# Kernel optimization log

Measured on AMD Instinct MI355X. Metric: run time of the kernel, lower is better.

## Reference

```python
import jax, jax.numpy as jnp
import numpy as np

N_HEAD = 16


def setup_inputs() -> dict:
    key = jax.random.key(0)
    k1, k2, k3 = jax.random.split(key, 3)
    B, T, C = 4, 2048, 1024
    x = jax.random.normal(k1, (B, T, C), dtype=jnp.float32)
    Wqkv = jax.random.normal(k2, (C, 3 * C), dtype=jnp.float32) * 0.02
    Wproj = jax.random.normal(k3, (C, C), dtype=jnp.float32) * 0.02
    return {"x": x, "Wqkv": Wqkv, "Wproj": Wproj}


def reference(x, Wqkv, Wproj):
    B, T, C = x.shape
    nh = N_HEAD
    hd = C // nh
    qkv = x @ Wqkv                                  # (B, T, 3C)
    q, k, v = jnp.split(qkv, 3, axis=-1)
    # (B, T, C) -> (B, nh, T, hd)
    q = q.reshape(B, T, nh, hd).transpose(0, 2, 1, 3)
    k = k.reshape(B, T, nh, hd).transpose(0, 2, 1, 3)
    v = v.reshape(B, T, nh, hd).transpose(0, 2, 1, 3)
    # scaled dot-product attention with causal mask (past_kv=None => T_all == T)
    att = jnp.einsum("bhtd,bhsd->bhts", q, k) / jnp.sqrt(jnp.float32(hd))
    causal = jnp.tril(jnp.ones((T, T), dtype=bool))  # (T, T)
    att = jnp.where(causal[None, None, :, :], att, jnp.float32(-jnp.inf))
    att = jax.nn.softmax(att, axis=-1)              # (B, nh, T, T)
    y = jnp.einsum("bhts,bhsd->bhtd", att, v)       # (B, nh, T, hd)
    y = y.transpose(0, 2, 1, 3).reshape(B, T, C)
    y = y @ Wproj                                   # (B, T, C)
    # present_kv (detached in original)
    return y, jax.lax.stop_gradient(k), jax.lax.stop_gradient(v)
```

## Files before the change

### kernel.cpp

```cpp
#include <hip/hip_runtime.h>
#include <hip/hip_bf16.h>


typedef __bf16 bf16;
typedef __attribute__((ext_vector_type(8))) __bf16 bf16x8;
typedef __attribute__((ext_vector_type(4))) __bf16 bf16x4;
typedef __attribute__((ext_vector_type(4))) float f32x4;

#define AS_G __attribute__((address_space(1)))
#define AS_L __attribute__((address_space(3)))

#define QSCALE 0.1803368801111204f

__device__ __forceinline__ void gld_lds16(const bf16* g, bf16* l) {
  __builtin_amdgcn_global_load_lds((const AS_G void*)g, (AS_L void*)l, 16, 0, 0);
}

__global__ __launch_bounds__(256) void k_cast(const float* __restrict__ in,
                                              bf16* __restrict__ out, int n) {
  int i = (blockIdx.x * 256 + threadIdx.x) * 8;
  if (i >= n) return;
  float4 a = *(const float4*)(in + i);
  float4 b = *(const float4*)(in + i + 4);
  bf16x8 o;
  o[0] = (bf16)a.x; o[1] = (bf16)a.y; o[2] = (bf16)a.z; o[3] = (bf16)a.w;
  o[4] = (bf16)b.x; o[5] = (bf16)b.y; o[6] = (bf16)b.z; o[7] = (bf16)b.w;
  *(bf16x8*)(out + i) = o;
}

__global__ __launch_bounds__(256) void k_transpose(const float* __restrict__ in,
                                                   bf16* __restrict__ out,
                                                   int K, int N) {
  __shared__ float tile[32][33];
  int bx = blockIdx.x * 32;
  int by = blockIdx.y * 32;
  int tx = threadIdx.x, ty = threadIdx.y;
#pragma unroll
  for (int i = 0; i < 4; ++i)
    tile[ty + i * 8][tx] = in[(size_t)(by + ty + i * 8) * N + bx + tx];
  __syncthreads();
#pragma unroll
  for (int i = 0; i < 4; ++i)
    out[(size_t)(bx + ty + i * 8) * K + by + tx] = (bf16)tile[tx][ty + i * 8];
}

__device__ __forceinline__ void gemm_tile_128(const bf16* __restrict__ A,
                                              const bf16* __restrict__ Bt,
                                              int m0, int n0,
                                              bf16* As, bf16* Bs,
                                              f32x4 acc[4][4]) {
  const int tid = threadIdx.x;
  const int w = tid >> 6, lane = tid & 63, lo = lane & 15, hi = lane >> 4;
  const int wm = w >> 1, wn = w & 1;
#pragma unroll 1
  for (int k0 = 0; k0 < 1024; k0 += 32) {
#pragma unroll
    for (int p = 0; p < 2; ++p) {
      int u = tid + 256 * p;
      int row = u >> 2, cs = u & 3;
      int g = cs ^ ((row >> 1) & 3);
      gld_lds16(A + (size_t)(m0 + row) * 1024 + k0 + g * 8, As + p * 2048 + w * 512);
      gld_lds16(Bt + (size_t)(n0 + row) * 1024 + k0 + g * 8, Bs + p * 2048 + w * 512);
    }
    __syncthreads();
    bf16x8 af[4], bfr[4];
#pragma unroll
    for (int i = 0; i < 4; ++i) {
      int row = wm * 64 + i * 16 + lo;
      af[i] = *(const bf16x8*)(As + row * 32 + (hi ^ ((row >> 1) & 3)) * 8);
    }
#pragma unroll
    for (int j = 0; j < 4; ++j) {
      int row = wn * 64 + j * 16 + lo;
      bfr[j] = *(const bf16x8*)(Bs + row * 32 + (hi ^ ((row >> 1) & 3)) * 8);
    }
#pragma unroll
    for (int i = 0; i < 4; ++i)
#pragma unroll
      for (int j = 0; j < 4; ++j)
        acc[i][j] = __builtin_amdgcn_mfma_f32_16x16x32_bf16(af[i], bfr[j], acc[i][j], 0, 0, 0);
    __syncthreads();
  }
}

__global__ __launch_bounds__(256) void k_gemm_qkv(const bf16* __restrict__ x,
                                                  const bf16* __restrict__ WqkvT,
                                                  bf16* __restrict__ qb, bf16* __restrict__ kb,
                                                  bf16* __restrict__ vtb,
                                                  float* __restrict__ outk, float* __restrict__ outv) {
  __shared__ bf16 As[128 * 32], Bs[128 * 32];
  f32x4 acc[4][4] = {};
  int m0 = blockIdx.y * 128, n0 = blockIdx.x * 128;
  gemm_tile_128(x, WqkvT, m0, n0, As, Bs, acc);
  const int tid = threadIdx.x;
  const int w = tid >> 6, lane = tid & 63, lo = lane & 15, hi = lane >> 4;
  const int wm = w >> 1, wn = w & 1;
#pragma unroll
  for (int i = 0; i < 4; ++i) {
    int growbase = m0 + wm * 64 + i * 16 + hi * 4;
    int b = growbase >> 11, t0 = growbase & 2047;
#pragma unroll
    for (int j = 0; j < 4; ++j) {
      int gcol = n0 + wn * 64 + j * 16 + lo;
      int part = gcol >> 10;
      int cc = gcol & 1023, h = cc >> 6, d = cc & 63;
      size_t idx0 = ((size_t)(b * 16 + h) * 2048 + t0) * 64 + d;
      if (part == 0) {
#pragma unroll
        for (int r = 0; r < 4; ++r) qb[idx0 + (size_t)r * 64] = (bf16)(acc[i][j][r] * QSCALE);
      } else if (part == 1) {
#pragma unroll
        for (int r = 0; r < 4; ++r) {
          float val = acc[i][j][r];
          kb[idx0 + (size_t)r * 64] = (bf16)val;
          outk[idx0 + (size_t)r * 64] = val;
        }
      } else {
        bf16x4 pk;
#pragma unroll
        for (int r = 0; r < 4; ++r) {
          float val = acc[i][j][r];
          outv[idx0 + (size_t)r * 64] = val;
          pk[r] = (bf16)val;
        }
        *(bf16x4*)(vtb + ((size_t)(b * 16 + h) * 64 + d) * 2048 + t0) = pk;
      }
    }
  }
}

__global__ __launch_bounds__(256) void k_gemm_proj(const bf16* __restrict__ yb,
                                                   const bf16* __restrict__ WprojT,
                                                   float* __restrict__ out) {
  __shared__ bf16 As[128 * 32], Bs[128 * 32];
  f32x4 acc[4][4] = {};
  int m0 = blockIdx.y * 128, n0 = blockIdx.x * 128;
  gemm_tile_128(yb, WprojT, m0, n0, As, Bs, acc);
  const int tid = threadIdx.x;
  const int w = tid >> 6, lane = tid & 63, lo = lane & 15, hi = lane >> 4;
  const int wm = w >> 1, wn = w & 1;
#pragma unroll
  for (int i = 0; i < 4; ++i)
#pragma unroll
    for (int j = 0; j < 4; ++j)
#pragma unroll
      for (int r = 0; r < 4; ++r) {
        int grow = m0 + wm * 64 + i * 16 + hi * 4 + r;
        int gcol = n0 + wn * 64 + j * 16 + lo;
        out[(size_t)grow * 1024 + gcol] = acc[i][j][r];
      }
}

__device__ __forceinline__ void p_store(f32x4 sacc[4], bool mask,
                                        int w, int lo, int hi, bf16* psrow) {
  if (mask) {
#pragma unroll
    for (int nt = 0; nt < 4; ++nt)
#pragma unroll
      for (int r = 0; r < 4; ++r)
        if (nt * 16 + hi * 4 + r > w * 16 + lo) sacc[nt][r] = -1e30f;
  }
#pragma unroll
  for (int nt = 0; nt < 4; ++nt) {
    bf16x4 pk;
#pragma unroll
    for (int r = 0; r < 4; ++r) pk[r] = (bf16)exp2f(sacc[nt][r]);
    *(bf16x4*)(psrow + (w * 16 + lo) * 72 + nt * 16 + hi * 4) = pk;
  }
}

__device__ __forceinline__ void write_y(bf16* __restrict__ y, int b, int h, int qrow,
                                        int hi, const f32x4 o[4], float inv) {
  size_t base = ((size_t)b * 2048 + qrow) * 1024 + h * 64;
#pragma unroll
  for (int mt = 0; mt < 4; ++mt) {
    bf16x4 yk;
#pragma unroll
    for (int r = 0; r < 4; ++r) yk[r] = (bf16)(o[mt][r] * inv);
    *(bf16x4*)(y + base + mt * 16 + hi * 4) = yk;
  }
}

__global__ __launch_bounds__(256, 4) void k_flash(const bf16* __restrict__ q,
                                                  const bf16* __restrict__ k,
                                                  const bf16* __restrict__ vt,
                                                  bf16* __restrict__ y) {
  __shared__ bf16 Ks[64 * 64];
  __shared__ bf16 Vs[80 * 64];
  __shared__ bf16 Ps[128 * 72];
  const int bi = blockIdx.x;
  const int slot = bi >> 3;
  const int bh = (bi & 7) + 8 * (slot >> 4);
  const int j = slot & 15;
  const int jA = j, jB = 31 - j;
  const int tid = threadIdx.x, w = tid >> 6, lane = tid & 63, lo = lane & 15, hi = lane >> 4;
  const bf16* qp = q + (size_t)bh * 2048 * 64;
  const bf16* kp = k + (size_t)bh * 2048 * 64;
  const bf16* vtp = vt + (size_t)bh * 64 * 2048;

  {
    int rr = tid >> 4, c = (tid & 15) * 4;
    bf16x4 z;
    bf16 v1 = (rr == 0) ? (bf16)1.0f : (bf16)0.0f;
    z[0] = v1; z[1] = v1; z[2] = v1; z[3] = v1;
    *(bf16x4*)(Vs + (64 + rr) * 64 + c) = z;
  }

  bf16x8 qfA[2], qfB[2];
  {
    int qA = jA * 64 + w * 16 + lo;
    int qB = jB * 64 + w * 16 + lo;
    qfA[0] = *(const bf16x8*)(qp + (size_t)qA * 64 + hi * 8);
    qfA[1] = *(const bf16x8*)(qp + (size_t)qA * 64 + 32 + hi * 8);
    qfB[0] = *(const bf16x8*)(qp + (size_t)qB * 64 + hi * 8);
    qfB[1] = *(const bf16x8*)(qp + (size_t)qB * 64 + 32 + hi * 8);
  }
  f32x4 oA[4] = {}, oB[4] = {};
  f32x4 oLA = {}, oLB = {};

  for (int st = 0; st <= jB; ++st) {
    const int s0 = st * 64;
#pragma unroll
    for (int p = 0; p < 2; ++p) {
      int u = tid + 256 * p;
      int row = u >> 3, c = u & 7, g = c ^ (row & 7);
      gld_lds16(kp + (size_t)(s0 + row) * 64 + g * 8, Ks + p * 2048 + w * 512);
      gld_lds16(vtp + (size_t)row * 2048 + s0 + g * 8, Vs + p * 2048 + w * 512);
    }
    __syncthreads();

    bf16x8 kf[4][2];
#pragma unroll
    for (int nt = 0; nt < 4; ++nt)
#pragma unroll
      for (int ks = 0; ks < 2; ++ks)
        kf[nt][ks] = *(const bf16x8*)(Ks + (nt * 16 + lo) * 64 + ((ks * 4 + hi) ^ (lo & 7)) * 8);

    const bool actA = (st <= jA);
    if (actA) {
      f32x4 sacc[4] = {};
#pragma unroll
      for (int nt = 0; nt < 4; ++nt)
#pragma unroll
        for (int ks = 0; ks < 2; ++ks)
          sacc[nt] = __builtin_amdgcn_mfma_f32_16x16x32_bf16(kf[nt][ks], qfA[ks], sacc[nt], 0, 0, 0);
      p_store(sacc, st == jA, w, lo, hi, Ps);
    }
    {
      f32x4 sacc[4] = {};
#pragma unroll
      for (int nt = 0; nt < 4; ++nt)
#pragma unroll
        for (int ks = 0; ks < 2; ++ks)
          sacc[nt] = __builtin_amdgcn_mfma_f32_16x16x32_bf16(kf[nt][ks], qfB[ks], sacc[nt], 0, 0, 0);
      p_store(sacc, st == jB, w, lo, hi, Ps + 64 * 72);
    }
    __asm__ volatile("s_waitcnt lgkmcnt(0)" ::: "memory");

    bf16x8 pfA[2], pfB[2];
#pragma unroll
    for (int ks = 0; ks < 2; ++ks) {
      pfB[ks] = *(const bf16x8*)(Ps + (64 + w * 16 + lo) * 72 + ks * 32 + hi * 8);
      if (actA) pfA[ks] = *(const bf16x8*)(Ps + (w * 16 + lo) * 72 + ks * 32 + hi * 8);
    }
#pragma unroll
    for (int mt = 0; mt < 5; ++mt) {
#pragma unroll
      for (int ks = 0; ks < 2; ++ks) {
        int row = mt * 16 + lo;
        bf16x8 vf = *(const bf16x8*)(Vs + row * 64 + ((ks * 4 + hi) ^ (row & 7)) * 8);
        if (mt < 4) {
          oB[mt] = __builtin_amdgcn_mfma_f32_16x16x32_bf16(vf, pfB[ks], oB[mt], 0, 0, 0);
          if (actA) oA[mt] = __builtin_amdgcn_mfma_f32_16x16x32_bf16(vf, pfA[ks], oA[mt], 0, 0, 0);
        } else {
          oLB = __builtin_amdgcn_mfma_f32_16x16x32_bf16(vf, pfB[ks], oLB, 0, 0, 0);
          if (actA) oLA = __builtin_amdgcn_mfma_f32_16x16x32_bf16(vf, pfA[ks], oLA, 0, 0, 0);
        }
      }
    }
    __syncthreads();
  }

  const int b = bh >> 4, h = bh & 15;
  float lA = __shfl(oLA[0], lo, 64);
  float lB = __shfl(oLB[0], lo, 64);
  write_y(y, b, h, jA * 64 + w * 16 + lo, hi, oA, 1.0f / lA);
  write_y(y, b, h, jB * 64 + w * 16 + lo, hi, oB, 1.0f / lB);
}

extern "C" void kernel_launch(void* const* d_in, const int* in_sizes, int n_in,
                              void* d_out, int out_size, void* d_ws, size_t ws_size,
                              hipStream_t stream) {
  const float* x = (const float*)d_in[0];
  const float* Wqkv = (const float*)d_in[1];
  const float* Wproj = (const float*)d_in[2];
  float* out = (float*)d_out;

  const size_t YSZ = (size_t)8192 * 1024;
  char* ws = (char*)d_ws;
  bf16* xb = (bf16*)ws;      ws += (size_t)8192 * 1024 * 2;
  bf16* wqkvT = (bf16*)ws;   ws += (size_t)3072 * 1024 * 2;
  bf16* wprojT = (bf16*)ws;  ws += (size_t)1024 * 1024 * 2;
  bf16* qb = (bf16*)ws;      ws += (size_t)64 * 2048 * 64 * 2;
  bf16* kb = (bf16*)ws;      ws += (size_t)64 * 2048 * 64 * 2;
  bf16* vtb = (bf16*)ws;     ws += (size_t)64 * 2048 * 64 * 2;
  bf16* yb = (bf16*)ws;

  float* outy = out;
  float* outk = out + YSZ;
  float* outv = out + 2 * YSZ;

  k_cast<<<4096, 256, 0, stream>>>(x, xb, 8388608);
  dim3 tb(32, 8);
  k_transpose<<<dim3(96, 32), tb, 0, stream>>>(Wqkv, wqkvT, 1024, 3072);
  k_transpose<<<dim3(32, 32), tb, 0, stream>>>(Wproj, wprojT, 1024, 1024);
  k_gemm_qkv<<<dim3(24, 64), 256, 0, stream>>>(xb, wqkvT, qb, kb, vtb, outk, outv);
  k_flash<<<1024, 256, 0, stream>>>(qb, kb, vtb, yb);
  k_gemm_proj<<<dim3(8, 64), 256, 0, stream>>>(yb, wprojT, outy);
}
```

Before: 324.3 us.

## Use 256x256 triple-buffered GEMM tiles and tweak flash attention P layout

Both projection GEMMs switch to 512-thread blocks computing 256x256 tiles. They use a three-stage LDS pipeline with split A/B prefetch, MFMA priority raising and an XCD-aware block swizzle, which raises data reuse and hides global load latency. The flash kernel pads the P scratch stride to cut LDS bank conflicts, uses the hardware exp2 builtin, and issues both score MFMA batches before the exp/stores. Bigger tiles leave the proj GEMM with only 128 blocks, which risks underfilling the GPU.

```diff
diff --git a/kernel.cpp b/kernel.cpp
--- a/kernel.cpp
+++ b/kernel.cpp
@@ -44,74 +44,112 @@
     out[(size_t)(bx + ty + i * 8) * K + by + tx] = (bf16)tile[tx][ty + i * 8];
 }
 
-__device__ __forceinline__ void gemm_tile_128(const bf16* __restrict__ A,
+__device__ __forceinline__ void gemm_main_256(const bf16* __restrict__ A,
                                               const bf16* __restrict__ Bt,
                                               int m0, int n0,
                                               bf16* As, bf16* Bs,
-                                              f32x4 acc[4][4]) {
+                                              f32x4 acc[8][4]) {
   const int tid = threadIdx.x;
   const int w = tid >> 6, lane = tid & 63, lo = lane & 15, hi = lane >> 4;
-  const int wm = w >> 1, wn = w & 1;
+  const int wm = w >> 2, wn = w & 3;
+  const int r0 = tid >> 2;
+  const int g = (tid & 3) ^ (r0 & 3) ^ ((r0 >> 2) & 3);
+  const bf16* ga = A + (size_t)(m0 + r0) * 1024 + g * 8;
+  const bf16* gb = Bt + (size_t)(n0 + r0) * 1024 + g * 8;
+
+#define STAGE_A(t, i) do { \
+    gld_lds16(ga + (t) * 32, As + (i) * 8192 + w * 512); \
+    gld_lds16(ga + 131072 + (t) * 32, As + (i) * 8192 + 4096 + w * 512); } while (0)
+#define STAGE_B(t, i) do { \
+    gld_lds16(gb + (t) * 32, Bs + (i) * 8192 + w * 512); \
+    gld_lds16(gb + 131072 + (t) * 32, Bs + (i) * 8192 + 4096 + w * 512); } while (0)
+
+  STAGE_A(0, 0); STAGE_B(0, 0);
+  STAGE_A(1, 1); STAGE_B(1, 1);
+
+  bf16x8 a[4], b[4];
 #pragma unroll 1
-  for (int k0 = 0; k0 < 1024; k0 += 32) {
-#pragma unroll
-    for (int p = 0; p < 2; ++p) {
-      int u = tid + 256 * p;
-      int row = u >> 2, cs = u & 3;
-      int g = cs ^ ((row >> 1) & 3);
-      gld_lds16(A + (size_t)(m0 + row) * 1024 + k0 + g * 8, As + p * 2048 + w * 512);
-      gld_lds16(Bt + (size_t)(n0 + row) * 1024 + k0 + g * 8, Bs + p * 2048 + w * 512);
-    }
-    __syncthreads();
-    bf16x8 af[4], bfr[4];
-#pragma unroll
-    for (int i = 0; i < 4; ++i) {
-      int row = wm * 64 + i * 16 + lo;
-      af[i] = *(const bf16x8*)(As + row * 32 + (hi ^ ((row >> 1) & 3)) * 8);
-    }
-#pragma unroll
-    for (int j = 0; j < 4; ++j) {
-      int row = wn * 64 + j * 16 + lo;
-      bfr[j] = *(const bf16x8*)(Bs + row * 32 + (hi ^ ((row >> 1) & 3)) * 8);
-    }
-#pragma unroll
-    for (int i = 0; i < 4; ++i)
-#pragma unroll
-      for (int j = 0; j < 4; ++j)
-        acc[i][j] = __builtin_amdgcn_mfma_f32_16x16x32_bf16(af[i], bfr[j], acc[i][j], 0, 0, 0);
-    __syncthreads();
-  }
-}
-
-__global__ __launch_bounds__(256) void k_gemm_qkv(const bf16* __restrict__ x,
-                                                  const bf16* __restrict__ WqkvT,
-                                                  bf16* __restrict__ qb, bf16* __restrict__ kb,
-                                                  bf16* __restrict__ vtb,
-                                                  float* __restrict__ outk, float* __restrict__ outv) {
-  __shared__ bf16 As[128 * 32], Bs[128 * 32];
-  f32x4 acc[4][4] = {};
-  int m0 = blockIdx.y * 128, n0 = blockIdx.x * 128;
-  gemm_tile_128(x, WqkvT, m0, n0, As, Bs, acc);
+  for (int t = 0; t < 32; ++t) {
+    if (t < 31) asm volatile("s_waitcnt vmcnt(4)" ::: "memory");
+    else        asm volatile("s_waitcnt vmcnt(0)" ::: "memory");
+    __builtin_amdgcn_s_barrier();
+    const int buf = t % 3;
+    const int sbuf = (t + 2) % 3;
+    const bf16* Ab = As + buf * 8192;
+    const bf16* Bb = Bs + buf * 8192;
+
+#pragma unroll
+    for (int mi = 0; mi < 4; ++mi) {
+      int r = wm * 128 + mi * 16 + lo;
+      a[mi] = *(const bf16x8*)(Ab + r * 32 + (hi ^ (r & 3) ^ ((r >> 2) & 3)) * 8);
+    }
+#pragma unroll
+    for (int ni = 0; ni < 4; ++ni) {
+      int r = wn * 64 + ni * 16 + lo;
+      b[ni] = *(const bf16x8*)(Bb + r * 32 + (hi ^ (r & 3) ^ ((r >> 2) & 3)) * 8);
+    }
+    if (t < 30) STAGE_A(t + 2, sbuf);
+    __builtin_amdgcn_s_barrier();
+    __builtin_amdgcn_s_setprio(1);
+#pragma unroll
+    for (int mi = 0; mi < 4; ++mi)
+#pragma unroll
+      for (int ni = 0; ni < 4; ++ni)
+        acc[mi][ni] = __builtin_amdgcn_mfma_f32_16x16x32_bf16(a[mi], b[ni], acc[mi][ni], 0, 0, 0);
+    __builtin_amdgcn_s_setprio(0);
+    __builtin_amdgcn_s_barrier();
+
+#pragma unroll
+    for (int mi = 0; mi < 4; ++mi) {
+      int r = wm * 128 + 64 + mi * 16 + lo;
+      a[mi] = *(const bf16x8*)(Ab + r * 32 + (hi ^ (r & 3) ^ ((r >> 2) & 3)) * 8);
+    }
+    if (t < 30) STAGE_B(t + 2, sbuf);
+    __builtin_amdgcn_s_barrier();
+    __builtin_amdgcn_s_setprio(1);
+#pragma unroll
+    for (int mi = 0; mi < 4; ++mi)
+#pragma unroll
+      for (int ni = 0; ni < 4; ++ni)
+        acc[4 + mi][ni] = __builtin_amdgcn_mfma_f32_16x16x32_bf16(a[mi], b[ni], acc[4 + mi][ni], 0, 0, 0);
+    __builtin_amdgcn_s_setprio(0);
+  }
+#undef STAGE_A
+#undef STAGE_B
+}
+
+__global__ __launch_bounds__(512, 2) void k_gemm_qkv(const bf16* __restrict__ x,
+                                                     const bf16* __restrict__ WqkvT,
+                                                     bf16* __restrict__ qb, bf16* __restrict__ kb,
+                                                     bf16* __restrict__ vtb,
+                                                     float* __restrict__ outk, float* __restrict__ outv) {
+  __shared__ bf16 As[3 * 8192], Bs[3 * 8192];
+  int id = blockIdx.x;
+  int swz = (id & 7) * 48 + (id >> 3);
+  int by = swz / 12, bx = swz - by * 12;
+  int m0 = by * 256, n0 = bx * 256;
+  f32x4 acc[8][4] = {};
+  gemm_main_256(x, WqkvT, m0, n0, As, Bs, acc);
   const int tid = threadIdx.x;
   const int w = tid >> 6, lane = tid & 63, lo = lane & 15, hi = lane >> 4;
-  const int wm = w >> 1, wn = w & 1;
-#pragma unroll
-  for (int i = 0; i < 4; ++i) {
-    int growbase = m0 + wm * 64 + i * 16 + hi * 4;
-    int b = growbase >> 11, t0 = growbase & 2047;
-#pragma unroll
-    for (int j = 0; j < 4; ++j) {
-      int gcol = n0 + wn * 64 + j * 16 + lo;
+  const int wm = w >> 2, wn = w & 3;
+#pragma unroll
+  for (int mi = 0; mi < 8; ++mi) {
+    int growbase = m0 + wm * 128 + mi * 16 + hi * 4;
+    int bb = growbase >> 11, t0 = growbase & 2047;
+#pragma unroll
+    for (int ni = 0; ni < 4; ++ni) {
+      int gcol = n0 + wn * 64 + ni * 16 + lo;
       int part = gcol >> 10;
       int cc = gcol & 1023, h = cc >> 6, d = cc & 63;
-      size_t idx0 = ((size_t)(b * 16 + h) * 2048 + t0) * 64 + d;
+      size_t idx0 = ((size_t)(bb * 16 + h) * 2048 + t0) * 64 + d;
       if (part == 0) {
 #pragma unroll
-        for (int r = 0; r < 4; ++r) qb[idx0 + (size_t)r * 64] = (bf16)(acc[i][j][r] * QSCALE);
+        for (int r = 0; r < 4; ++r) qb[idx0 + (size_t)r * 64] = (bf16)(acc[mi][ni][r] * QSCALE);
       } else if (part == 1) {
 #pragma unroll
         for (int r = 0; r < 4; ++r) {
-          float val = acc[i][j][r];
+          float val = acc[mi][ni][r];
           kb[idx0 + (size_t)r * 64] = (bf16)val;
           outk[idx0 + (size_t)r * 64] = val;
         }
@@ -119,37 +157,42 @@
         bf16x4 pk;
 #pragma unroll
         for (int r = 0; r < 4; ++r) {
-          float val = acc[i][j][r];
+          float val = acc[mi][ni][r];
           outv[idx0 + (size_t)r * 64] = val;
           pk[r] = (bf16)val;
         }
-        *(bf16x4*)(vtb + ((size_t)(b * 16 + h) * 64 + d) * 2048 + t0) = pk;
+        *(bf16x4*)(vtb + ((size_t)(bb * 16 + h) * 64 + d) * 2048 + t0) = pk;
       }
     }
   }
 }
 
-__global__ __launch_bounds__(256) void k_gemm_proj(const bf16* __restrict__ yb,
-                                                   const bf16* __restrict__ WprojT,
-                                                   float* __restrict__ out) {
-  __shared__ bf16 As[128 * 32], Bs[128 * 32];
-  f32x4 acc[4][4] = {};
-  int m0 = blockIdx.y * 128, n0 = blockIdx.x * 128;
-  gemm_tile_128(yb, WprojT, m0, n0, As, Bs, acc);
+__global__ __launch_bounds__(512, 2) void k_gemm_proj(const bf16* __restrict__ yb,
+                                                      const bf16* __restrict__ WprojT,
+                                                      float* __restrict__ out) {
+  __shared__ bf16 As[3 * 8192], Bs[3 * 8192];
+  int id = blockIdx.x;
+  int swz = (id & 7) * 16 + (id >> 3);
+  int by = swz >> 2, bx = swz & 3;
+  int m0 = by * 256, n0 = bx * 256;
+  f32x4 acc[8][4] = {};
+  gemm_main_256(yb, WprojT, m0, n0, As, Bs, acc);
   const int tid = threadIdx.x;
   const int w = tid >> 6, lane = tid & 63, lo = lane & 15, hi = lane >> 4;
-  const int wm = w >> 1, wn = w & 1;
-#pragma unroll
-  for (int i = 0; i < 4; ++i)
-#pragma unroll
-    for (int j = 0; j < 4; ++j)
+  const int wm = w >> 2, wn = w & 3;
+#pragma unroll
+  for (int mi = 0; mi < 8; ++mi)
+#pragma unroll
+    for (int ni = 0; ni < 4; ++ni)
 #pragma unroll
       for (int r = 0; r < 4; ++r) {
-        int grow = m0 + wm * 64 + i * 16 + hi * 4 + r;
-        int gcol = n0 + wn * 64 + j * 16 + lo;
-        out[(size_t)grow * 1024 + gcol] = acc[i][j][r];
+        int grow = m0 + wm * 128 + mi * 16 + hi * 4 + r;
+        int gcol = n0 + wn * 64 + ni * 16 + lo;
+        out[(size_t)grow * 1024 + gcol] = acc[mi][ni][r];
       }
 }
+
+#define PSTR 76
 
 __device__ __forceinline__ void p_store(f32x4 sacc[4], bool mask,
                                         int w, int lo, int hi, bf16* psrow) {
@@ -164,8 +207,8 @@
   for (int nt = 0; nt < 4; ++nt) {
     bf16x4 pk;
 #pragma unroll
-    for (int r = 0; r < 4; ++r) pk[r] = (bf16)exp2f(sacc[nt][r]);
-    *(bf16x4*)(psrow + (w * 16 + lo) * 72 + nt * 16 + hi * 4) = pk;
+    for (int r = 0; r < 4; ++r) pk[r] = (bf16)__builtin_amdgcn_exp2f(sacc[nt][r]);
+    *(bf16x4*)(psrow + (w * 16 + lo) * PSTR + nt * 16 + hi * 4) = pk;
   }
 }
 
@@ -187,7 +230,7 @@
                                                   bf16* __restrict__ y) {
   __shared__ bf16 Ks[64 * 64];
   __shared__ bf16 Vs[80 * 64];
-  __shared__ bf16 Ps[128 * 72];
+  __shared__ bf16 Ps[128 * PSTR];
   const int bi = blockIdx.x;
   const int slot = bi >> 3;
   const int bh = (bi & 7) + 8 * (slot >> 4);
@@ -237,31 +280,28 @@
         kf[nt][ks] = *(const bf16x8*)(Ks + (nt * 16 + lo) * 64 + ((ks * 4 + hi) ^ (lo & 7)) * 8);
 
     const bool actA = (st <= jA);
+    f32x4 saccA[4] = {}, saccB[4] = {};
     if (actA) {
-      f32x4 sacc[4] = {};
 #pragma unroll
       for (int nt = 0; nt < 4; ++nt)
 #pragma unroll
         for (int ks = 0; ks < 2; ++ks)
-          sacc[nt] = __builtin_amdgcn_mfma_f32_16x16x32_bf16(kf[nt][ks], qfA[ks], sacc[nt], 0, 0, 0);
-      p_store(sacc, st == jA, w, lo, hi, Ps);
-    }
-    {
-      f32x4 sacc[4] = {};
-#pragma unroll
-      for (int nt = 0; nt < 4; ++nt)
-#pragma unroll
-        for (int ks = 0; ks < 2; ++ks)
-          sacc[nt] = __builtin_amdgcn_mfma_f32_16x16x32_bf16(kf[nt][ks], qfB[ks], sacc[nt], 0, 0, 0);
-      p_store(sacc, st == jB, w, lo, hi, Ps + 64 * 72);
-    }
+          saccA[nt] = __builtin_amdgcn_mfma_f32_16x16x32_bf16(kf[nt][ks], qfA[ks], saccA[nt], 0, 0, 0);
+    }
+#pragma unroll
+    for (int nt = 0; nt < 4; ++nt)
+#pragma unroll
+      for (int ks = 0; ks < 2; ++ks)
+        saccB[nt] = __builtin_amdgcn_mfma_f32_16x16x32_bf16(kf[nt][ks], qfB[ks], saccB[nt], 0, 0, 0);
+    if (actA) p_store(saccA, st == jA, w, lo, hi, Ps);
+    p_store(saccB, st == jB, w, lo, hi, Ps + 64 * PSTR);
     __asm__ volatile("s_waitcnt lgkmcnt(0)" ::: "memory");
 
     bf16x8 pfA[2], pfB[2];
 #pragma unroll
     for (int ks = 0; ks < 2; ++ks) {
-      pfB[ks] = *(const bf16x8*)(Ps + (64 + w * 16 + lo) * 72 + ks * 32 + hi * 8);
-      if (actA) pfA[ks] = *(const bf16x8*)(Ps + (w * 16 + lo) * 72 + ks * 32 + hi * 8);
+      pfB[ks] = *(const bf16x8*)(Ps + (64 + w * 16 + lo) * PSTR + ks * 32 + hi * 8);
+      if (actA) pfA[ks] = *(const bf16x8*)(Ps + (w * 16 + lo) * PSTR + ks * 32 + hi * 8);
     }
 #pragma unroll
     for (int mt = 0; mt < 5; ++mt) {
@@ -314,7 +354,7 @@
   dim3 tb(32, 8);
   k_transpose<<<dim3(96, 32), tb, 0, stream>>>(Wqkv, wqkvT, 1024, 3072);
   k_transpose<<<dim3(32, 32), tb, 0, stream>>>(Wproj, wprojT, 1024, 1024);
-  k_gemm_qkv<<<dim3(24, 64), 256, 0, stream>>>(xb, wqkvT, qb, kb, vtb, outk, outv);
+  k_gemm_qkv<<<384, 512, 0, stream>>>(xb, wqkvT, qb, kb, vtb, outk, outv);
   k_flash<<<1024, 256, 0, stream>>>(qb, kb, vtb, yb);
-  k_gemm_proj<<<dim3(8, 64), 256, 0, stream>>>(yb, wprojT, outy);
-}
+  k_gemm_proj<<<128, 512, 0, stream>>>(yb, wprojT, outy);
+}
```

After: 321.5 us. About the same (-0.9%).
